# Kernel tuning notes

Measured on AMD Instinct MI355X. Metric: run time of the kernel, lower is better.

## Reference

```python
import jax, jax.numpy as jnp
import numpy as np
from jax import lax

DEPTH, STACKS = 8, 2
C, SK, OUT = 64, 256, 256          # res_channels, skip_channels, out_channels
NB = DEPTH * STACKS                 # 16 blocks
DILS = [2 ** i for i in range(DEPTH)] * STACKS


def causal_conv(x, w, dil):
    # x: [B,C,T], w: [2C,C,2]; causal: left-pad by dil, kernel size 2 dilated
    return lax.conv_general_dilated(
        x, w, window_strides=(1,), padding=[(dil, 0)], rhs_dilation=(dil,),
        dimension_numbers=('NCH', 'OIH', 'NCH'))


def conv1x1(x, w):
    # x: [B,c_in,T], w: [c_out,c_in]
    return jnp.einsum('oc,bct->bot', w, x)


def setup_inputs() -> dict:
    key = jax.random.key(0)
    ks = jax.random.split(key, 8)
    B, T = 4, 8192
    x = jax.random.randint(ks[0], (B, T), 0, 256)
    h = jax.random.normal(ks[1], (B, NB * 2 * C, T), dtype=jnp.float32)
    embed = jax.random.normal(ks[2], (256, C), dtype=jnp.float32) * 0.1
    w_conv = jax.random.normal(ks[3], (NB, 2 * C, C, 2), dtype=jnp.float32) * 0.08
    w_res = jax.random.normal(ks[4], (NB, C, C), dtype=jnp.float32) * 0.08
    w_skip = jax.random.normal(ks[5], (NB, SK, C), dtype=jnp.float32) * 0.08
    w_out1 = jax.random.normal(ks[6], (OUT, SK), dtype=jnp.float32) * 0.05
    w_out2 = jax.random.normal(ks[7], (OUT, OUT), dtype=jnp.float32) * 0.05
    return {'x': x, 'h': h, 'embed': embed, 'w_conv': w_conv,
            'w_res': w_res, 'w_skip': w_skip, 'w_out1': w_out1, 'w_out2': w_out2}


def reference(x, h, embed, w_conv, w_res, w_skip, w_out1, w_out2):
    out = embed[x].transpose(0, 2, 1)          # [B,C,T]
    hs = jnp.split(h, NB, axis=1)              # NB chunks of [B,2C,T]
    skip = None
    for i in range(NB):
        g = causal_conv(out, w_conv[i], DILS[i]) + hs[i]   # [B,2C,T]
        z = jnp.tanh(g[:, :C]) * jax.nn.sigmoid(g[:, C:])  # gated activation
        s = conv1x1(z, w_skip[i])                          # [B,SK,T]
        skip = s if skip is None else skip + s
        if i < NB - 1:  # last block has return_residual=False (skip only)
            out = out + conv1x1(z, w_res[i])
    y = jax.nn.relu(skip)
    y = jax.nn.relu(conv1x1(y, w_out1))
    return conv1x1(y, w_out2)                  # [B,OUT,T]
```

## Files before the change

### kernel.cpp

```cpp
#include <hip/hip_runtime.h>

#define NB 16
#define TT 8192
#define Bb 4

typedef __attribute__((ext_vector_type(8))) short short8;
typedef __attribute__((ext_vector_type(16))) float f32x16;

__device__ __forceinline__ unsigned short bf16_rn(float f) {
  unsigned int u = __float_as_uint(f);
  u += 0x7FFF + ((u >> 16) & 1);
  return (unsigned short)(u >> 16);
}
__device__ __forceinline__ unsigned int pack2(float a, float b) {
  return (unsigned int)bf16_rn(a) | ((unsigned int)bf16_rn(b) << 16);
}
__device__ __forceinline__ int kpos(int k) {
  int g = (k >> 2) & 1;
  int e = (k & 3) + 4 * (k >> 3);
  return g * 8 + e;
}
__device__ __forceinline__ int kinv(int p) {
  int g = p >> 3, e = p & 7;
  return (e & 3) + 4 * g + 8 * (e >> 2);
}

#define WINRD(base, r, off)                                                    \
  (*(const short8*)((char*)(base) +                                            \
      (((unsigned int)((r) * 128 + (off) * 2)) ^                               \
       ((unsigned int)(((r) & 7) << 4)))))

__global__ __launch_bounds__(256) void prep_weights(
    const float* __restrict__ wconv, const float* __restrict__ wres,
    const float* __restrict__ wsk, const float* __restrict__ w1,
    const float* __restrict__ w2, short* __restrict__ dwc,
    short* __restrict__ dwr, short* __restrict__ dws,
    short* __restrict__ dw1, short* __restrict__ dw2)
{
  int i = blockIdx.x * 256 + threadIdx.x;
  if (i < 262144) {
    int k = kinv(i & 15);
    int ic = (i & 48) | k;
    int oc = (i >> 6) & 127;
    int tap = (i >> 13) & 1;
    int blk = i >> 14;
    dwc[i] = (short)bf16_rn(wconv[(((blk * 128 + oc) * 64 + ic) << 1) | tap]);
    return;
  }
  int j = i - 262144;
  if (j < 65536) { dwr[j] = (short)bf16_rn(wres[(j & ~15) | kinv(j & 15)]); return; }
  j -= 65536;
  if (j < 262144) { dws[j] = (short)bf16_rn(wsk[(j & ~15) | kinv(j & 15)]); return; }
  j -= 262144;
  if (j < 65536) { dw1[j] = (short)bf16_rn(w1[(j & ~15) | kinv(j & 15)]); return; }
  j -= 65536;
  if (j < 65536) { dw2[j] = (short)bf16_rn(w2[(j & ~15) | kinv(j & 15)]); return; }
}

__global__ __launch_bounds__(256, 4) void block_kernel(
    const float* __restrict__ rin, float* __restrict__ rout,
    const int* __restrict__ x, const float* __restrict__ embed,
    const float* __restrict__ h, const short* __restrict__ wc,
    const short* __restrict__ wr, unsigned short* __restrict__ zg,
    int blk, int dil, int last)
{
  __shared__ short win[2][160 * 64];
  __shared__ float rs[2][32 * 64];
  __shared__ short zl[2][32 * 64];

  const int b = blockIdx.y;
  const int tile = threadIdx.x >> 7;
  const int htid = threadIdx.x & 127;
  const int t0 = (blockIdx.x * 2 + tile) * 32;
  const int lane = htid & 63, wv = htid >> 6;
  const int l31 = lane & 31, hi = lane >> 5;

  short* winT = win[tile];
  float* rsT = rs[tile];
  short* zlT = zl[tile];

  const int tcol = t0 + l31;
  f32x16 aA, aS;
  const float* hb = h + ((size_t)b * 2048 + (size_t)blk * 128) * TT;
#pragma unroll
  for (int r = 0; r < 16; ++r) {
    int row = (r & 3) + 4 * hi + 8 * (r >> 2) + 32 * wv;
    aA[r] = hb[(size_t)row * TT + tcol];
    aS[r] = hb[(size_t)(row + 64) * TT + tcol];
  }

  if (blk == 0) {
    const int* xb = x + b * TT;
#pragma unroll
    for (int it = 0; it < 8; ++it) {
      int u = it * 128 + htid;
      int cpair = u & 31, t = u >> 5;
      int c0 = cpair * 2;
      int xi = xb[t0 + t];
      float v0 = embed[(size_t)xi * 64 + c0];
      float v1 = embed[(size_t)xi * 64 + c0 + 1];
      rsT[t * 64 + c0] = v0;
      rsT[t * 64 + c0 + 1] = v1;
      int p0 = (c0 & 48) | kpos(c0 & 15);
      int w = dil + t;
      unsigned int byte = (unsigned int)(w * 128 + p0 * 2) ^
                          (unsigned int)((w & 7) << 4);
      *(unsigned int*)((char*)winT + byte) = pack2(v0, v1);
    }
    if (htid < 32) {
      int c0 = htid * 2;
      float v0 = 0.f, v1 = 0.f;
      if (t0 > 0) {
        int xi = xb[t0 - 1];
        v0 = embed[(size_t)xi * 64 + c0];
        v1 = embed[(size_t)xi * 64 + c0 + 1];
      }
      int p0 = (c0 & 48) | kpos(c0 & 15);
      unsigned int byte = (unsigned int)(p0 * 2);
      *(unsigned int*)((char*)winT + byte) = pack2(v0, v1);
    }
  } else {
    const float* rbase = rin + (size_t)b * TT * 64;
#pragma unroll
    for (int it = 0; it < 8; ++it) {
      int u = it * 128 + htid;
      int cpair = u & 31, t = u >> 5;
      int c0 = cpair * 2;
      float2 f = *(const float2*)(rbase + (size_t)(t0 + t) * 64 + c0);
      rsT[t * 64 + c0] = f.x;
      rsT[t * 64 + c0 + 1] = f.y;
      int p0 = (c0 & 48) | kpos(c0 & 15);
      int w = dil + t;
      unsigned int byte = (unsigned int)(w * 128 + p0 * 2) ^
                          (unsigned int)((w & 7) << 4);
      *(unsigned int*)((char*)winT + byte) = pack2(f.x, f.y);
    }
    for (int u = htid; u < dil * 32; u += 128) {
      int cpair = u & 31, w = u >> 5;
      int c0 = cpair * 2;
      int gt = t0 - dil + w;
      float2 f = {0.f, 0.f};
      if (gt >= 0) f = *(const float2*)(rbase + (size_t)gt * 64 + c0);
      int p0 = (c0 & 48) | kpos(c0 & 15);
      unsigned int byte = (unsigned int)(w * 128 + p0 * 2) ^
                          (unsigned int)((w & 7) << 4);
      *(unsigned int*)((char*)winT + byte) = pack2(f.x, f.y);
    }
  }
  __syncthreads();

  const short* wA0 = wc + (size_t)blk * 16384 + (32 * wv + l31) * 64;
  const short* wA1 = wA0 + 8192;
  const int r1 = dil + l31;
  const int r0 = l31;
#pragma unroll
  for (int ks = 0; ks < 4; ++ks) {
    int off = ks * 16 + 8 * hi;
    short8 b1 = WINRD(winT, r1, off);
    short8 b0 = WINRD(winT, r0, off);
    short8 a0t = *(const short8*)(wA0 + off);
    short8 a1t = *(const short8*)(wA1 + off);
    short8 a0s = *(const short8*)(wA0 + 4096 + off);
    short8 a1s = *(const short8*)(wA1 + 4096 + off);
    aA = __builtin_amdgcn_mfma_f32_32x32x16_bf16(a0t, b0, aA, 0, 0, 0);
    aA = __builtin_amdgcn_mfma_f32_32x32x16_bf16(a1t, b1, aA, 0, 0, 0);
    aS = __builtin_amdgcn_mfma_f32_32x32x16_bf16(a0s, b0, aS, 0, 0, 0);
    aS = __builtin_amdgcn_mfma_f32_32x32x16_bf16(a1s, b1, aS, 0, 0, 0);
  }

#pragma unroll
  for (int r = 0; r < 16; r += 2) {
    int ic0 = (r & 3) + 4 * hi + 8 * (r >> 2) + 32 * wv;
    float z0 = (1.f - 2.f / (__expf(2.f * aA[r]) + 1.f)) *
               (1.f / (1.f + __expf(-aS[r])));
    float z1 = (1.f - 2.f / (__expf(2.f * aA[r + 1]) + 1.f)) *
               (1.f / (1.f + __expf(-aS[r + 1])));
    int p = (ic0 & ~15) | kpos(ic0 & 15);
    int tloc = l31;
    unsigned int byte = (unsigned int)(tloc * 128 + p * 2) ^
                        (unsigned int)((tloc & 7) << 4);
    *(unsigned int*)((char*)zlT + byte) = pack2(z0, z1);
  }
  __syncthreads();

  {
    unsigned short* zb = zg + ((size_t)(blk * Bb + b) * TT + t0) * 64;
#pragma unroll
    for (int it = 0; it < 8; ++it) {
      int u = it * 128 + htid;
      int p2 = u & 31, t = u >> 5;
      unsigned int byte = (unsigned int)(t * 128 + p2 * 4) ^
                          (unsigned int)((t & 7) << 4);
      unsigned int v = *(const unsigned int*)((char*)zlT + byte);
      *(unsigned int*)(zb + (size_t)t * 64 + p2 * 2) = v;
    }
  }

  if (!last) {
    const int trow = l31;
    f32x16 ar = {};
    const short* wrb = wr + (size_t)blk * 4096 + (wv * 32 + l31) * 64;
#pragma unroll
    for (int ks = 0; ks < 4; ++ks) {
      int off = ks * 16 + 8 * hi;
      short8 az = WINRD(zlT, trow, off);
      short8 bw = *(const short8*)(wrb + off);
      ar = __builtin_amdgcn_mfma_f32_32x32x16_bf16(az, bw, ar, 0, 0, 0);
    }
    float* obase = rout + (size_t)b * TT * 64;
    int oc = wv * 32 + l31;
#pragma unroll
    for (int r = 0; r < 16; ++r) {
      int t = (r & 3) + 4 * hi + 8 * (r >> 2);
      obase[(size_t)(t0 + t) * 64 + oc] = rsT[t * 64 + oc] + ar[r];
    }
  }
}

__global__ __launch_bounds__(256) void head_kernel(
    const unsigned short* __restrict__ zg, const short* __restrict__ wsk,
    const short* __restrict__ w1, const short* __restrict__ w2,
    float* __restrict__ out)
{
  __shared__ short zbuf[2][32 * 64];
  __shared__ short yb[32 * 256];
  __shared__ short y2b[32 * 256];

  const int b = blockIdx.y;
  const int t0 = blockIdx.x * 32;
  const int tid = threadIdx.x;
  const int lane = tid & 63, wv = tid >> 6;
  const int l31 = lane & 31, hi = lane >> 5;

  {
#pragma unroll
    for (int it = 0; it < 4; ++it) {
      int u = it * 256 + tid;
      int p2 = u & 31, t = u >> 5;
      unsigned int v = *(const unsigned int*)(zg +
          ((size_t)(0 * Bb + b) * TT + t0 + t) * 64 + p2 * 2);
      unsigned int byte = (unsigned int)(t * 128 + p2 * 4) ^
                          (unsigned int)((t & 7) << 4);
      *(unsigned int*)((char*)zbuf[0] + byte) = v;
    }
  }

  f32x16 acc0 = {}, acc1 = {};
  const short* wsb0 = wsk + (wv * 32 + l31) * 64;
  const short* wsb1 = wsk + ((wv + 4) * 32 + l31) * 64;

  for (int blk = 0; blk < NB; ++blk) {
    __syncthreads();
    if (blk < NB - 1) {
#pragma unroll
      for (int it = 0; it < 4; ++it) {
        int u = it * 256 + tid;
        int p2 = u & 31, t = u >> 5;
        unsigned int v = *(const unsigned int*)(zg +
            ((size_t)((blk + 1) * Bb + b) * TT + t0 + t) * 64 + p2 * 2);
        unsigned int byte = (unsigned int)(t * 128 + p2 * 4) ^
                            (unsigned int)((t & 7) << 4);
        *(unsigned int*)((char*)zbuf[(blk + 1) & 1] + byte) = v;
      }
    }
    const short* zb = zbuf[blk & 1];
#pragma unroll
    for (int ks = 0; ks < 4; ++ks) {
      int off = ks * 16 + 8 * hi;
      short8 bw0 = *(const short8*)(wsb0 + (size_t)blk * 16384 + off);
      short8 bw1 = *(const short8*)(wsb1 + (size_t)blk * 16384 + off);
      short8 az = WINRD(zb, l31, off);
      acc0 = __builtin_amdgcn_mfma_f32_32x32x16_bf16(az, bw0, acc0, 0, 0, 0);
      acc1 = __builtin_amdgcn_mfma_f32_32x32x16_bf16(az, bw1, acc1, 0, 0, 0);
    }
  }

  {
    int sk0 = wv * 32 + l31;
    int sk1 = sk0 + 128;
    int p0 = (sk0 & 0xF0) | kpos(sk0 & 15);
    int p1 = (sk1 & 0xF0) | kpos(sk1 & 15);
#pragma unroll
    for (int r = 0; r < 16; ++r) {
      int dt = (r & 3) + 4 * hi + 8 * (r >> 2);
      unsigned int b0 = (unsigned int)(dt * 512 + p0 * 2) ^
                        (unsigned int)((dt & 7) << 4);
      unsigned int b1 = (unsigned int)(dt * 512 + p1 * 2) ^
                        (unsigned int)((dt & 7) << 4);
      *(short*)((char*)yb + b0) = (short)bf16_rn(fmaxf(acc0[r], 0.f));
      *(short*)((char*)yb + b1) = (short)bf16_rn(fmaxf(acc1[r], 0.f));
    }
  }
  __syncthreads();

#pragma unroll
  for (int ot = 0; ot < 2; ++ot) {
    const short* w1r = w1 + ((wv + 4 * ot) * 32 + l31) * 256;
    const int trow = l31;
    f32x16 acc = {};
#pragma unroll
    for (int ks = 0; ks < 16; ++ks) {
      int off = ks * 16 + 8 * hi;
      short8 by = *(const short8*)((char*)yb +
          ((unsigned int)(trow * 512 + off * 2) ^ (unsigned int)((trow & 7) << 4)));
      short8 aw = *(const short8*)(w1r + off);
      acc = __builtin_amdgcn_mfma_f32_32x32x16_bf16(aw, by, acc, 0, 0, 0);
    }
#pragma unroll
    for (int r = 0; r < 16; r += 2) {
      int o0 = (wv + 4 * ot) * 32 + (r & 3) + 4 * hi + 8 * (r >> 2);
      unsigned int v = (unsigned int)bf16_rn(fmaxf(acc[r], 0.f)) |
                       ((unsigned int)bf16_rn(fmaxf(acc[r + 1], 0.f)) << 16);
      int p = (o0 & 0xF0) | kpos(o0 & 15);
      unsigned int byte = (unsigned int)(trow * 512 + p * 2) ^
                          (unsigned int)((trow & 7) << 4);
      *(unsigned int*)((char*)y2b + byte) = v;
    }
  }
  __syncthreads();

  {
    float* ob = out + (size_t)b * 256 * TT;
#pragma unroll
    for (int ot = 0; ot < 2; ++ot) {
      const short* w2r = w2 + ((wv + 4 * ot) * 32 + l31) * 256;
      const int trow = l31;
      f32x16 acc = {};
#pragma unroll
      for (int ks = 0; ks < 16; ++ks) {
        int off = ks * 16 + 8 * hi;
        short8 by = *(const short8*)((char*)y2b +
            ((unsigned int)(trow * 512 + off * 2) ^ (unsigned int)((trow & 7) << 4)));
        short8 aw = *(const short8*)(w2r + off);
        acc = __builtin_amdgcn_mfma_f32_32x32x16_bf16(aw, by, acc, 0, 0, 0);
      }
#pragma unroll
      for (int r = 0; r < 16; ++r) {
        int oc = (wv + 4 * ot) * 32 + (r & 3) + 4 * hi + 8 * (r >> 2);
        ob[(size_t)oc * TT + t0 + trow] = acc[r];
      }
    }
  }
}

extern "C" void kernel_launch(void* const* d_in, const int* in_sizes, int n_in,
                              void* d_out, int out_size, void* d_ws, size_t ws_size,
                              hipStream_t stream)
{
  const int* x = (const int*)d_in[0];
  const float* h = (const float*)d_in[1];
  const float* embed = (const float*)d_in[2];
  const float* w_conv = (const float*)d_in[3];
  const float* w_res = (const float*)d_in[4];
  const float* w_skip = (const float*)d_in[5];
  const float* w_out1 = (const float*)d_in[6];
  const float* w_out2 = (const float*)d_in[7];
  float* out = (float*)d_out;

  char* ws = (char*)d_ws;
  float* r0 = (float*)ws;
  float* r1 = (float*)(ws + (size_t)(8 << 20));
  unsigned short* zg = (unsigned short*)(ws + (size_t)(16 << 20));
  short* dwc = (short*)(ws + (size_t)(80 << 20));
  short* dwr = dwc + 262144;
  short* dws = dwr + 65536;
  short* dw1 = dws + 262144;
  short* dw2 = dw1 + 65536;

  prep_weights<<<2816, 256, 0, stream>>>(w_conv, w_res, w_skip, w_out1, w_out2,
                                         dwc, dwr, dws, dw1, dw2);

  float* rf[2] = {r0, r1};
  const int dils[NB] = {1, 2, 4, 8, 16, 32, 64, 128,
                        1, 2, 4, 8, 16, 32, 64, 128};
  for (int i = 0; i < NB; ++i) {
    block_kernel<<<dim3(TT / 64, Bb), 256, 0, stream>>>(
        rf[i & 1], rf[(i + 1) & 1], x, embed, h, dwc, dwr, zg,
        i, dils[i], i == NB - 1);
  }

  head_kernel<<<dim3(TT / 32, Bb), 256, 0, stream>>>(zg, dws, dw1, dw2, out);
}
```

Measured before the change: 368.3 us.

## Fuse consecutive residual blocks into one kernel using halo-recompute windows

Replaces sixteen per-block launches with four fused kernels. Each processes several dilated blocks for a 128-step tile, keeping the residual in LDS and recomputing a left halo (64 or 192 extra steps) so the causal dependencies stay local. This removes the per-block global round trips of the residual stream and the launch overhead. In exchange it does redundant conv/gate work on the halo, reloads h for the halo columns, and uses larger LDS footprints with 512-thread blocks, which may lower occupancy.

```diff
diff --git a/kernel.cpp b/kernel.cpp
--- a/kernel.cpp
+++ b/kernel.cpp
@@ -57,163 +57,195 @@
   if (j < 65536) { dw2[j] = (short)bf16_rn(w2[(j & ~15) | kinv(j & 15)]); return; }
 }
 
-__global__ __launch_bounds__(256, 4) void block_kernel(
+template <int BLK0, int NBLK, int W, int NCT, int MAXT, int FIRSTK, int LASTK>
+__global__ __launch_bounds__(512) void fused_kernel(
     const float* __restrict__ rin, float* __restrict__ rout,
     const int* __restrict__ x, const float* __restrict__ embed,
     const float* __restrict__ h, const short* __restrict__ wc,
-    const short* __restrict__ wr, unsigned short* __restrict__ zg,
-    int blk, int dil, int last)
+    const short* __restrict__ wr, unsigned short* __restrict__ zg)
 {
-  __shared__ short win[2][160 * 64];
-  __shared__ float rs[2][32 * 64];
-  __shared__ short zl[2][32 * 64];
+  __shared__ float rs[W * 64];
+  __shared__ short wz[W * 64];
 
   const int b = blockIdx.y;
-  const int tile = threadIdx.x >> 7;
-  const int htid = threadIdx.x & 127;
-  const int t0 = (blockIdx.x * 2 + tile) * 32;
-  const int lane = htid & 63, wv = htid >> 6;
+  const int t0 = blockIdx.x * 128;
+  const int t0m = t0 - (W - 128);
+  const int tid = threadIdx.x;
+  const int lane = tid & 63, wv = tid >> 6;
   const int l31 = lane & 31, hi = lane >> 5;
 
-  short* winT = win[tile];
-  float* rsT = rs[tile];
-  short* zlT = zl[tile];
-
-  const int tcol = t0 + l31;
-  f32x16 aA, aS;
-  const float* hb = h + ((size_t)b * 2048 + (size_t)blk * 128) * TT;
-#pragma unroll
-  for (int r = 0; r < 16; ++r) {
-    int row = (r & 3) + 4 * hi + 8 * (r >> 2) + 32 * wv;
-    aA[r] = hb[(size_t)row * TT + tcol];
-    aS[r] = hb[(size_t)(row + 64) * TT + tcol];
-  }
-
-  if (blk == 0) {
+  if (FIRSTK) {
     const int* xb = x + b * TT;
-#pragma unroll
-    for (int it = 0; it < 8; ++it) {
-      int u = it * 128 + htid;
-      int cpair = u & 31, t = u >> 5;
-      int c0 = cpair * 2;
-      int xi = xb[t0 + t];
-      float v0 = embed[(size_t)xi * 64 + c0];
-      float v1 = embed[(size_t)xi * 64 + c0 + 1];
-      rsT[t * 64 + c0] = v0;
-      rsT[t * 64 + c0 + 1] = v1;
-      int p0 = (c0 & 48) | kpos(c0 & 15);
-      int w = dil + t;
-      unsigned int byte = (unsigned int)(w * 128 + p0 * 2) ^
-                          (unsigned int)((w & 7) << 4);
-      *(unsigned int*)((char*)winT + byte) = pack2(v0, v1);
-    }
-    if (htid < 32) {
-      int c0 = htid * 2;
+    for (int u = tid; u < W * 32; u += 512) {
+      int cpair = u & 31, w = u >> 5, c0 = cpair * 2;
+      int gt = t0m + w;
       float v0 = 0.f, v1 = 0.f;
-      if (t0 > 0) {
-        int xi = xb[t0 - 1];
+      if (gt >= 0) {
+        int xi = xb[gt];
         v0 = embed[(size_t)xi * 64 + c0];
         v1 = embed[(size_t)xi * 64 + c0 + 1];
       }
-      int p0 = (c0 & 48) | kpos(c0 & 15);
-      unsigned int byte = (unsigned int)(p0 * 2);
-      *(unsigned int*)((char*)winT + byte) = pack2(v0, v1);
-    }
-  } else {
-    const float* rbase = rin + (size_t)b * TT * 64;
-#pragma unroll
-    for (int it = 0; it < 8; ++it) {
-      int u = it * 128 + htid;
-      int cpair = u & 31, t = u >> 5;
-      int c0 = cpair * 2;
-      float2 f = *(const float2*)(rbase + (size_t)(t0 + t) * 64 + c0);
-      rsT[t * 64 + c0] = f.x;
-      rsT[t * 64 + c0 + 1] = f.y;
-      int p0 = (c0 & 48) | kpos(c0 & 15);
-      int w = dil + t;
-      unsigned int byte = (unsigned int)(w * 128 + p0 * 2) ^
-                          (unsigned int)((w & 7) << 4);
-      *(unsigned int*)((char*)winT + byte) = pack2(f.x, f.y);
-    }
-    for (int u = htid; u < dil * 32; u += 128) {
-      int cpair = u & 31, w = u >> 5;
-      int c0 = cpair * 2;
-      int gt = t0 - dil + w;
-      float2 f = {0.f, 0.f};
-      if (gt >= 0) f = *(const float2*)(rbase + (size_t)gt * 64 + c0);
+      rs[w * 64 + c0] = v0;
+      rs[w * 64 + c0 + 1] = v1;
       int p0 = (c0 & 48) | kpos(c0 & 15);
       unsigned int byte = (unsigned int)(w * 128 + p0 * 2) ^
                           (unsigned int)((w & 7) << 4);
-      *(unsigned int*)((char*)winT + byte) = pack2(f.x, f.y);
+      *(unsigned int*)((char*)wz + byte) = pack2(v0, v1);
+    }
+  } else {
+    const float* rbase = rin + (size_t)b * TT * 64;
+    for (int u = tid; u < W * 16; u += 512) {
+      int q = u & 15, w = u >> 4, c0 = q * 4;
+      int gt = t0m + w;
+      float4 f = {0.f, 0.f, 0.f, 0.f};
+      if (gt >= 0) f = *(const float4*)(rbase + (size_t)gt * 64 + c0);
+      *(float4*)(rs + w * 64 + c0) = f;
+      int pa = (c0 & 48) | kpos(c0 & 15);
+      int pb = ((c0 + 2) & 48) | kpos((c0 + 2) & 15);
+      unsigned int sw = (unsigned int)((w & 7) << 4);
+      *(unsigned int*)((char*)wz + (((unsigned int)(w * 128 + pa * 2)) ^ sw)) =
+          pack2(f.x, f.y);
+      *(unsigned int*)((char*)wz + (((unsigned int)(w * 128 + pb * 2)) ^ sw)) =
+          pack2(f.z, f.w);
     }
   }
   __syncthreads();
 
-  const short* wA0 = wc + (size_t)blk * 16384 + (32 * wv + l31) * 64;
-  const short* wA1 = wA0 + 8192;
-  const int r1 = dil + l31;
-  const int r0 = l31;
-#pragma unroll
-  for (int ks = 0; ks < 4; ++ks) {
-    int off = ks * 16 + 8 * hi;
-    short8 b1 = WINRD(winT, r1, off);
-    short8 b0 = WINRD(winT, r0, off);
-    short8 a0t = *(const short8*)(wA0 + off);
-    short8 a1t = *(const short8*)(wA1 + off);
-    short8 a0s = *(const short8*)(wA0 + 4096 + off);
-    short8 a1s = *(const short8*)(wA1 + 4096 + off);
-    aA = __builtin_amdgcn_mfma_f32_32x32x16_bf16(a0t, b0, aA, 0, 0, 0);
-    aA = __builtin_amdgcn_mfma_f32_32x32x16_bf16(a1t, b1, aA, 0, 0, 0);
-    aS = __builtin_amdgcn_mfma_f32_32x32x16_bf16(a0s, b0, aS, 0, 0, 0);
-    aS = __builtin_amdgcn_mfma_f32_32x32x16_bf16(a1s, b1, aS, 0, 0, 0);
-  }
-
-#pragma unroll
-  for (int r = 0; r < 16; r += 2) {
-    int ic0 = (r & 3) + 4 * hi + 8 * (r >> 2) + 32 * wv;
-    float z0 = (1.f - 2.f / (__expf(2.f * aA[r]) + 1.f)) *
-               (1.f / (1.f + __expf(-aS[r])));
-    float z1 = (1.f - 2.f / (__expf(2.f * aA[r + 1]) + 1.f)) *
-               (1.f / (1.f + __expf(-aS[r + 1])));
-    int p = (ic0 & ~15) | kpos(ic0 & 15);
-    int tloc = l31;
-    unsigned int byte = (unsigned int)(tloc * 128 + p * 2) ^
-                        (unsigned int)((tloc & 7) << 4);
-    *(unsigned int*)((char*)zlT + byte) = pack2(z0, z1);
-  }
-  __syncthreads();
-
-  {
-    unsigned short* zb = zg + ((size_t)(blk * Bb + b) * TT + t0) * 64;
-#pragma unroll
-    for (int it = 0; it < 8; ++it) {
-      int u = it * 128 + htid;
-      int p2 = u & 31, t = u >> 5;
-      unsigned int byte = (unsigned int)(t * 128 + p2 * 4) ^
-                          (unsigned int)((t & 7) << 4);
-      unsigned int v = *(const unsigned int*)((char*)zlT + byte);
-      *(unsigned int*)(zb + (size_t)t * 64 + p2 * 2) = v;
-    }
-  }
-
-  if (!last) {
-    const int trow = l31;
-    f32x16 ar = {};
-    const short* wrb = wr + (size_t)blk * 4096 + (wv * 32 + l31) * 64;
-#pragma unroll
-    for (int ks = 0; ks < 4; ++ks) {
-      int off = ks * 16 + 8 * hi;
-      short8 az = WINRD(zlT, trow, off);
-      short8 bw = *(const short8*)(wrb + off);
-      ar = __builtin_amdgcn_mfma_f32_32x32x16_bf16(az, bw, ar, 0, 0, 0);
-    }
-    float* obase = rout + (size_t)b * TT * 64;
-    int oc = wv * 32 + l31;
-#pragma unroll
-    for (int r = 0; r < 16; ++r) {
-      int t = (r & 3) + 4 * hi + 8 * (r >> 2);
-      obase[(size_t)(t0 + t) * 64 + oc] = rsT[t * 64 + oc] + ar[r];
-    }
+  for (int j = 0; j < NBLK; ++j) {
+    const int blk = BLK0 + j;
+    const int dil = 1 << (blk & 7);
+    const bool lastg = (LASTK && j == NBLK - 1);
+    const bool lastj = (j == NBLK - 1);
+
+    unsigned int zp[MAXT][8];
+    const float* hb = h + ((size_t)b * 2048 + (size_t)blk * 128) * TT;
+#pragma unroll
+    for (int k = 0; k < MAXT; ++k) {
+      int id = wv + k * 8;
+      if (id < 2 * NCT) {
+        int ct = id >> 1, pr = id & 1;
+        int c = t0m + ct * 32 + l31;
+        int hc = c < 0 ? 0 : c;
+        f32x16 aA, aS;
+#pragma unroll
+        for (int r = 0; r < 16; ++r) {
+          int row = (r & 3) + 4 * hi + 8 * (r >> 2) + 32 * pr;
+          aA[r] = hb[(size_t)row * TT + hc];
+          aS[r] = hb[(size_t)(row + 64) * TT + hc];
+        }
+        const short* wA0 = wc + (size_t)blk * 16384 + (32 * pr + l31) * 64;
+        const short* wA1 = wA0 + 8192;
+        int r1w = ct * 32 + l31;
+        int r0w = r1w - dil; if (r0w < 0) r0w = 0;
+#pragma unroll
+        for (int ks = 0; ks < 4; ++ks) {
+          int off = ks * 16 + 8 * hi;
+          short8 b1 = WINRD(wz, r1w, off);
+          short8 b0 = WINRD(wz, r0w, off);
+          short8 a0t = *(const short8*)(wA0 + off);
+          short8 a1t = *(const short8*)(wA1 + off);
+          short8 a0s = *(const short8*)(wA0 + 4096 + off);
+          short8 a1s = *(const short8*)(wA1 + 4096 + off);
+          aA = __builtin_amdgcn_mfma_f32_32x32x16_bf16(a0t, b0, aA, 0, 0, 0);
+          aA = __builtin_amdgcn_mfma_f32_32x32x16_bf16(a1t, b1, aA, 0, 0, 0);
+          aS = __builtin_amdgcn_mfma_f32_32x32x16_bf16(a0s, b0, aS, 0, 0, 0);
+          aS = __builtin_amdgcn_mfma_f32_32x32x16_bf16(a1s, b1, aS, 0, 0, 0);
+        }
+#pragma unroll
+        for (int r = 0; r < 16; r += 2) {
+          float z0 = (1.f - 2.f / (__expf(2.f * aA[r]) + 1.f)) *
+                     (1.f / (1.f + __expf(-aS[r])));
+          float z1 = (1.f - 2.f / (__expf(2.f * aA[r + 1]) + 1.f)) *
+                     (1.f / (1.f + __expf(-aS[r + 1])));
+          zp[k][r >> 1] = pack2(z0, z1);
+        }
+      }
+    }
+    __syncthreads();
+
+#pragma unroll
+    for (int k = 0; k < MAXT; ++k) {
+      int id = wv + k * 8;
+      if (id < 2 * NCT) {
+        int ct = id >> 1, pr = id & 1;
+        int w = ct * 32 + l31;
+        unsigned int sw = (unsigned int)((w & 7) << 4);
+#pragma unroll
+        for (int r = 0; r < 16; r += 2) {
+          int ic0 = (r & 3) + 4 * hi + 8 * (r >> 2) + 32 * pr;
+          int p = (ic0 & ~15) | kpos(ic0 & 15);
+          *(unsigned int*)((char*)wz + (((unsigned int)(w * 128 + p * 2)) ^ sw)) =
+              zp[k][r >> 1];
+        }
+      }
+    }
+    __syncthreads();
+
+    if (!lastg) {
+#pragma unroll
+      for (int k = 0; k < MAXT; ++k) {
+        int id = wv + k * 8;
+        if (id < 2 * NCT) {
+          int mt = id >> 1, ntr = id & 1;
+          int trow = mt * 32 + l31;
+          f32x16 ar = {};
+          const short* wrb = wr + (size_t)blk * 4096 + (ntr * 32 + l31) * 64;
+#pragma unroll
+          for (int ks = 0; ks < 4; ++ks) {
+            int off = ks * 16 + 8 * hi;
+            short8 az = WINRD(wz, trow, off);
+            short8 bw = *(const short8*)(wrb + off);
+            ar = __builtin_amdgcn_mfma_f32_32x32x16_bf16(az, bw, ar, 0, 0, 0);
+          }
+          int oc = ntr * 32 + l31;
+#pragma unroll
+          for (int r = 0; r < 16; ++r) {
+            int w = mt * 32 + (r & 3) + 4 * hi + 8 * (r >> 2);
+            rs[w * 64 + oc] += ar[r];
+          }
+        }
+      }
+    }
+    __syncthreads();
+
+    {
+      unsigned short* zb = zg + ((size_t)(blk * Bb + b) * TT + t0) * 64;
+#pragma unroll
+      for (int it = 0; it < 8; ++it) {
+        int u = it * 512 + tid;
+        int p2 = u & 31, t = u >> 5;
+        int w = (W - 128) + t;
+        unsigned int byte = (unsigned int)(w * 128 + p2 * 4) ^
+                            (unsigned int)((w & 7) << 4);
+        unsigned int v = *(const unsigned int*)((char*)wz + byte);
+        *(unsigned int*)(zb + (size_t)t * 64 + p2 * 2) = v;
+      }
+    }
+    __syncthreads();
+
+    if (!lastj) {
+      for (int u = tid; u < W * 32; u += 512) {
+        int cpair = u & 31, w = u >> 5, c0 = cpair * 2;
+        int gt = t0m + w;
+        float v0 = 0.f, v1 = 0.f;
+        if (gt >= 0) { v0 = rs[w * 64 + c0]; v1 = rs[w * 64 + c0 + 1]; }
+        int p0 = (c0 & 48) | kpos(c0 & 15);
+        unsigned int byte = (unsigned int)(w * 128 + p0 * 2) ^
+                            (unsigned int)((w & 7) << 4);
+        *(unsigned int*)((char*)wz + byte) = pack2(v0, v1);
+      }
+    } else if (!LASTK) {
+      float* ob = rout + (size_t)b * TT * 64;
+#pragma unroll
+      for (int it = 0; it < 4; ++it) {
+        int u = it * 512 + tid;
+        int q = u & 15, t = u >> 4;
+        int w = (W - 128) + t;
+        *(float4*)(ob + (size_t)(t0 + t) * 64 + q * 4) =
+            *(const float4*)(rs + w * 64 + q * 4);
+      }
+    }
+    __syncthreads();
   }
 }
 
@@ -370,14 +402,15 @@
   prep_weights<<<2816, 256, 0, stream>>>(w_conv, w_res, w_skip, w_out1, w_out2,
                                          dwc, dwr, dws, dw1, dw2);
 
-  float* rf[2] = {r0, r1};
-  const int dils[NB] = {1, 2, 4, 8, 16, 32, 64, 128,
-                        1, 2, 4, 8, 16, 32, 64, 128};
-  for (int i = 0; i < NB; ++i) {
-    block_kernel<<<dim3(TT / 64, Bb), 256, 0, stream>>>(
-        rf[i & 1], rf[(i + 1) & 1], x, embed, h, dwc, dwr, zg,
-        i, dils[i], i == NB - 1);
-  }
+  const dim3 grid(TT / 128, Bb);
+  fused_kernel<0, 6, 192, 6, 2, 1, 0><<<grid, 512, 0, stream>>>(
+      r1, r0, x, embed, h, dwc, dwr, zg);
+  fused_kernel<6, 2, 320, 10, 3, 0, 0><<<grid, 512, 0, stream>>>(
+      r0, r1, x, embed, h, dwc, dwr, zg);
+  fused_kernel<8, 6, 192, 6, 2, 0, 0><<<grid, 512, 0, stream>>>(
+      r1, r0, x, embed, h, dwc, dwr, zg);
+  fused_kernel<14, 2, 320, 10, 3, 0, 1><<<grid, 512, 0, stream>>>(
+      r0, r1, x, embed, h, dwc, dwr, zg);
 
   head_kernel<<<dim3(TT / 32, Bb), 256, 0, stream>>>(zg, dws, dw1, dw2, out);
 }
```

Measured after the change: 399.5 us. 8.5% more time.
